# Performance work log

Measured on AMD Instinct MI355X. Metric: run time of the kernel, lower is better.

Reference implementation:

```python
import jax, jax.numpy as jnp
import numpy as np

NQ, BS, HW, D, H, DFF = 300, 16, 2048, 256, 8, 2048
HD2 = (2 * D) // H   # cross-attn head dim (query/key), 64
VHD = D // H         # value head dim, 32
EPS = 1e-5


def _lin_params(key, din, dout):
    kw, kb = jax.random.split(key)
    w = jax.random.normal(kw, (din, dout), jnp.float32) * 0.02
    b = jax.random.normal(kb, (dout,), jnp.float32) * 0.02
    return w, b


def setup_inputs() -> dict:
    key = jax.random.key(0)
    ks = jax.random.split(key, 24)
    inp = {
        'tgt': jax.random.normal(ks[0], (NQ, BS, D), jnp.float32),
        'memory': jax.random.normal(ks[1], (HW, BS, D), jnp.float32),
        'pos': jax.random.normal(ks[2], (HW, BS, D), jnp.float32),
        'cls_query_pos': jax.random.normal(ks[3], (NQ, BS, D), jnp.float32),
        'cls_query_sine_embed': jax.random.normal(ks[4], (NQ, BS, D), jnp.float32),
    }
    names = [('w_qc', 'b_qc', D, D), ('w_qp', 'b_qp', D, D), ('w_kc', 'b_kc', D, D),
             ('w_kp', 'b_kp', D, D), ('w_v', 'b_v', D, D), ('w_qs', 'b_qs', D, D),
             ('wq', 'bq', 2 * D, 2 * D), ('wk', 'bk', 2 * D, 2 * D),
             ('wv', 'bv', D, D), ('wo', 'bo', D, D),
             ('w1', 'b1', D, DFF), ('w2', 'b2', DFF, D)]
    for i, (wn, bn, din, dout) in enumerate(names):
        w, b = _lin_params(ks[5 + i], din, dout)
        inp[wn], inp[bn] = w, b
    inp['g2'] = jnp.ones((D,), jnp.float32)
    inp['be2'] = jnp.zeros((D,), jnp.float32)
    inp['g3'] = jnp.ones((D,), jnp.float32)
    inp['be3'] = jnp.zeros((D,), jnp.float32)
    return inp


def _ln(x, g, b):
    m = x.mean(-1, keepdims=True)
    v = ((x - m) ** 2).mean(-1, keepdims=True)
    return (x - m) * jax.lax.rsqrt(v + EPS) * g + b


def reference(tgt, memory, pos, cls_query_pos, cls_query_sine_embed,
              w_qc, b_qc, w_qp, b_qp, w_kc, b_kc, w_kp, b_kp, w_v, b_v,
              w_qs, b_qs, wq, bq, wk, bk, wv, bv, wo, bo,
              w1, b1, w2, b2, g2, be2, g3, be3):
    nq, bs, d = tgt.shape
    hw = memory.shape[0]
    # conditional cross-attention projections (is_first=True path)
    q_content = tgt @ w_qc + b_qc
    k_content = memory @ w_kc + b_kc
    v_in = memory @ w_v + b_v
    k_pos = pos @ w_kp + b_kp
    q_pos = cls_query_pos @ w_qp + b_qp
    q = (q_content + q_pos).reshape(nq, bs, H, d // H)
    sine = (cls_query_sine_embed @ w_qs + b_qs).reshape(nq, bs, H, d // H)
    q = jnp.concatenate([q, sine], axis=3).reshape(nq, bs, 2 * d)
    k = (k_content + k_pos).reshape(hw, bs, H, d // H)
    kp = k_pos.reshape(hw, bs, H, d // H)
    k = jnp.concatenate([k, kp], axis=3).reshape(hw, bs, 2 * d)
    # MultiheadAttention(embed_dim=2d, nhead, vdim=d): internal q/k/v/out projs
    scale = 1.0 / jnp.sqrt(jnp.float32(HD2))
    qh = ((q @ wq + bq) * scale).reshape(nq, bs, H, HD2)
    kh = (k @ wk + bk).reshape(hw, bs, H, HD2)
    vh = (v_in @ wv + bv).reshape(hw, bs, H, VHD)
    logits = jnp.einsum('qbhd,kbhd->bhqk', qh, kh)
    attn = jax.nn.softmax(logits, axis=-1)              # [bs, H, nq, hw]
    ctx = jnp.einsum('bhqk,kbhd->qbhd', attn, vh).reshape(nq, bs, d)
    tgt2 = ctx @ wo + bo
    attn_avg = attn.mean(axis=1)                        # averaged over heads
    # residual + norm + FFN + norm (dropout disabled / eval)
    x = _ln(tgt + tgt2, g2, be2)
    ffn = jax.nn.relu(x @ w1 + b1) @ w2 + b2
    x = _ln(x + ffn, g3, be3)
    return (x, attn_avg)
```

## Files before the change

### kernel.cpp

```cpp
#include <hip/hip_runtime.h>

typedef unsigned short u16;
typedef __attribute__((ext_vector_type(8))) short short8;
typedef __attribute__((ext_vector_type(4))) float f32x4;

#define MFMA16(a, b, c) __builtin_amdgcn_mfma_f32_16x16x32_bf16(a, b, c, 0, 0, 0)

__device__ __forceinline__ float bf2f(u16 u) {
    return __uint_as_float(((unsigned)u) << 16);
}
__device__ __forceinline__ u16 f2bf(float f) {
    unsigned u = __float_as_uint(f);
    u += 0x7fff + ((u >> 16) & 1);
    return (u16)(u >> 16);
}

__global__ __launch_bounds__(256) void cvt2(const float* __restrict__ a,
                                            const float* __restrict__ b,
                                            u16* __restrict__ A, u16* __restrict__ B) {
    size_t i = ((size_t)blockIdx.x * 256 + threadIdx.x) * 4;
    float4 va = *(const float4*)(a + i);
    float4 vb = *(const float4*)(b + i);
    u16 ta[4] = {f2bf(va.x), f2bf(va.y), f2bf(va.z), f2bf(va.w)};
    u16 tb[4] = {f2bf(vb.x), f2bf(vb.y), f2bf(vb.z), f2bf(vb.w)};
    *(uint2*)(A + i) = *(uint2*)ta;
    *(uint2*)(B + i) = *(uint2*)tb;
}


__global__ __launch_bounds__(256) void fold_q(const float* __restrict__ w_qc,
                                              const float* __restrict__ w_qp,
                                              const float* __restrict__ w_qs,
                                              const float* __restrict__ wq,
                                              u16* __restrict__ WQ3T) {
    int o = blockIdx.x * 256 + threadIdx.x;
    int k0 = blockIdx.y * 4;
    int seg = k0 >> 8, kb = k0 & 255;
    const float* wsrc = (seg == 0) ? w_qc : ((seg == 1) ? w_qp : w_qs);
    int sOff = (seg == 2) ? 32 : 0;
    const float* wcol = wq + o;
    float acc[4] = {0.f, 0.f, 0.f, 0.f};
#pragma unroll 8
    for (int c = 0; c < 256; c++) {
        int mc = (c >> 5) * 64 + (c & 31) + sOff;
        float w0 = wcol[(size_t)mc * 512];
#pragma unroll
        for (int j = 0; j < 4; j++)
            acc[j] += wsrc[(size_t)(kb + j) * 256 + c] * w0;
    }
    u16 outv[4];
#pragma unroll
    for (int j = 0; j < 4; j++) outv[j] = f2bf(acc[j] * 0.125f);
    *(uint2*)(WQ3T + (size_t)o * 768 + k0) = *(uint2*)outv;
}

__global__ __launch_bounds__(256) void fold_k(const float* __restrict__ w_kc,
                                              const float* __restrict__ w_kp,
                                              const float* __restrict__ wk,
                                              u16* __restrict__ WK2T) {
    int o = blockIdx.x * 256 + threadIdx.x;
    int k0 = blockIdx.y * 4;
    bool second = k0 >= 256;
    int kb = second ? k0 - 256 : k0;
    const float* wcol = wk + o;
    float acc[4] = {0.f, 0.f, 0.f, 0.f};
    if (second) {
#pragma unroll 8
        for (int c = 0; c < 256; c++) {
            int mc = (c >> 5) * 64 + (c & 31);
            float w0 = wcol[(size_t)mc * 512] + wcol[(size_t)(mc + 32) * 512];
#pragma unroll
            for (int j = 0; j < 4; j++)
                acc[j] += w_kp[(size_t)(kb + j) * 256 + c] * w0;
        }
    } else {
#pragma unroll 8
        for (int c = 0; c < 256; c++) {
            int mc = (c >> 5) * 64 + (c & 31);
            float w0 = wcol[(size_t)mc * 512];
#pragma unroll
            for (int j = 0; j < 4; j++)
                acc[j] += w_kc[(size_t)(kb + j) * 256 + c] * w0;
        }
    }
    u16 outv[4];
#pragma unroll
    for (int j = 0; j < 4; j++) outv[j] = f2bf(acc[j]);
    *(uint2*)(WK2T + (size_t)o * 512 + k0) = *(uint2*)outv;
}

__global__ __launch_bounds__(256) void fold_v(const float* __restrict__ w_v,
                                              const float* __restrict__ wv_w,
                                              u16* __restrict__ WV2T) {
    int o = threadIdx.x;
    int k0 = blockIdx.y * 4;
    float acc[4] = {0.f, 0.f, 0.f, 0.f};
#pragma unroll 8
    for (int c = 0; c < 256; c++) {
        float w0 = wv_w[(size_t)c * 256 + o];
#pragma unroll
        for (int j = 0; j < 4; j++)
            acc[j] += w_v[(size_t)(k0 + j) * 256 + c] * w0;
    }
    u16 outv[4];
#pragma unroll
    for (int j = 0; j < 4; j++) outv[j] = f2bf(acc[j]);
    *(uint2*)(WV2T + (size_t)o * 256 + k0) = *(uint2*)outv;
}

__global__ __launch_bounds__(256) void fold_bias(
    const float* b_qc, const float* b_qp, const float* b_qs, const float* wq, const float* bq,
    const float* b_kc, const float* b_kp, const float* wk, const float* bk,
    const float* b_v, const float* wv_w, const float* bv,
    float* BQF, float* BKF, float* BVF) {
    __shared__ float red[4][64];
    int tid = threadIdx.x, lane = tid & 63, wave = tid >> 6;
    int blk = blockIdx.x;
    float acc = 0.f;
    if (blk < 8) {
        int o = blk * 64 + lane;
#pragma unroll 4
        for (int c = wave * 64; c < wave * 64 + 64; c++) {
            int mc = (c >> 5) * 64 + (c & 31);
            acc += (b_qc[c] + b_qp[c]) * wq[(size_t)mc * 512 + o];
            acc += b_qs[c] * wq[(size_t)(mc + 32) * 512 + o];
        }
        red[wave][lane] = acc;
        __syncthreads();
        if (wave == 0)
            BQF[o] = (bq[o] + red[0][lane] + red[1][lane] + red[2][lane] + red[3][lane]) * 0.125f;
    } else if (blk < 16) {
        int o = (blk - 8) * 64 + lane;
#pragma unroll 4
        for (int c = wave * 64; c < wave * 64 + 64; c++) {
            int mc = (c >> 5) * 64 + (c & 31);
            acc += (b_kc[c] + b_kp[c]) * wk[(size_t)mc * 512 + o];
            acc += b_kp[c] * wk[(size_t)(mc + 32) * 512 + o];
        }
        red[wave][lane] = acc;
        __syncthreads();
        if (wave == 0)
            BKF[o] = bk[o] + red[0][lane] + red[1][lane] + red[2][lane] + red[3][lane];
    } else {
        int o = (blk - 16) * 64 + lane;
#pragma unroll 4
        for (int c = wave * 64; c < wave * 64 + 64; c++)
            acc += b_v[c] * wv_w[(size_t)c * 256 + o];
        red[wave][lane] = acc;
        __syncthreads();
        if (wave == 0)
            BVF[o] = bv[o] + red[0][lane] + red[1][lane] + red[2][lane] + red[3][lane];
    }
}

__global__ __launch_bounds__(256) void transpose_f2b(const float* __restrict__ src,
                                                     u16* __restrict__ dst, int R, int C) {
    __shared__ float tile[32][33];
    int c0 = blockIdx.x * 32, r0 = blockIdx.y * 32;
    int t = threadIdx.x;
    int j = t & 31, i0 = (t >> 5) * 4;
#pragma unroll
    for (int ii = 0; ii < 4; ii++)
        tile[i0 + ii][j] = src[(size_t)(r0 + i0 + ii) * C + c0 + j];
    __syncthreads();
    int i2 = t & 31, j0 = (t >> 5) * 4;
#pragma unroll
    for (int jj = 0; jj < 4; jj++)
        dst[(size_t)(c0 + j0 + jj) * R + r0 + i2] = f2bf(tile[i2][j0 + jj]);
}

#define APAD 40
__global__ __launch_bounds__(256) void gemm_bt(
    const void* __restrict__ A0v, const void* __restrict__ A1v, const void* __restrict__ A2v,
    int astride, int a_f32, const u16* __restrict__ BT, const float* __restrict__ bias,
    u16* __restrict__ C, int M, int N, int K, int mode) {
    __shared__ u16 As[128 * APAD];
    __shared__ u16 Bs[128 * APAD];
    int tid = threadIdx.x;
    int wave = tid >> 6, lane = tid & 63;
    int l15 = lane & 15, quad = lane >> 4;
    int wm = (wave >> 1) * 64, wn = (wave & 1) * 64;
    int gm0 = blockIdx.x * 128, gn0 = blockIdx.y * 128;
    f32x4 acc[4][4] = {};
    for (int k0 = 0; k0 < K; k0 += 32) {
        const void* ap;
        int kin;
        if (astride == 256) {
            int p = k0 >> 8;
            ap = (p == 0) ? A0v : ((p == 1) ? A1v : A2v);
            kin = k0 & 255;
        } else {
            ap = A0v;
            kin = k0;
        }
#pragma unroll
        for (int i = 0; i < 2; i++) {
            int idx = tid * 2 + i;
            int row = idx >> 2, seg = (idx & 3) * 8;
            int grow = gm0 + row;
            u16 tmp[8];
            if (a_f32) {
                float vv[8] = {0.f, 0.f, 0.f, 0.f, 0.f, 0.f, 0.f, 0.f};
                if (grow < M) {
                    const float* apf = (const float*)ap;
                    float4 u0 = *(const float4*)(apf + (size_t)grow * astride + kin + seg);
                    float4 u1 = *(const float4*)(apf + (size_t)grow * astride + kin + seg + 4);
                    vv[0] = u0.x; vv[1] = u0.y; vv[2] = u0.z; vv[3] = u0.w;
                    vv[4] = u1.x; vv[5] = u1.y; vv[6] = u1.z; vv[7] = u1.w;
                }
#pragma unroll
                for (int e = 0; e < 8; e++) tmp[e] = f2bf(vv[e]);
            } else {
                uint4 v;
                v.x = v.y = v.z = v.w = 0;
                if (grow < M) v = *(const uint4*)((const u16*)ap + (size_t)grow * astride + kin + seg);
                *(uint4*)tmp = v;
            }
            *(uint4*)(&As[row * APAD + seg]) = *(uint4*)tmp;
            int nrow = gn0 + row;
            uint4 w = *(const uint4*)(BT + (size_t)nrow * K + k0 + seg);
            *(uint4*)(&Bs[row * APAD + seg]) = w;
        }
        __syncthreads();
        short8 afr[4], bfr[4];
#pragma unroll
        for (int i = 0; i < 4; i++)
            afr[i] = *(const short8*)(&As[(wm + i * 16 + l15) * APAD + quad * 8]);
#pragma unroll
        for (int j = 0; j < 4; j++)
            bfr[j] = *(const short8*)(&Bs[(wn + j * 16 + l15) * APAD + quad * 8]);
#pragma unroll
        for (int i = 0; i < 4; i++)
#pragma unroll
            for (int j = 0; j < 4; j++) acc[i][j] = MFMA16(afr[i], bfr[j], acc[i][j]);
        __syncthreads();
    }
#pragma unroll
    for (int i = 0; i < 4; i++) {
        int row = gm0 + wm + i * 16 + quad * 4;
#pragma unroll
        for (int j = 0; j < 4; j++) {
            int col = gn0 + wn + j * 16 + l15;
            float bvv = bias[col];
#pragma unroll
            for (int r = 0; r < 4; r++) {
                int grow = row + r;
                if (grow < M) {
                    float v = acc[i][j][r] + bvv;
                    if (mode == 1) v = fmaxf(v, 0.f);
                    C[(size_t)grow * N + col] = f2bf(v);
                }
            }
        }
    }
}

__global__ __launch_bounds__(256) void attn_a(const u16* __restrict__ qh,
                                              const u16* __restrict__ kh,
                                              const u16* __restrict__ vhr,
                                              u16* __restrict__ ctxbuf,
                                              float* __restrict__ z8inv) {
    int qt = blockIdx.x, h = blockIdx.y, b = blockIdx.z;
    __shared__ u16 Qt[64 * 72];
    __shared__ u16 Kc[128 * 72];
    __shared__ u16 Pt[64 * 136];
    __shared__ u16 VTc[32 * 136];
    int tid = threadIdx.x, wave = tid >> 6, lane = tid & 63;
    int l15 = lane & 15, quad = lane >> 4;
    int q0 = qt * 64;
#pragma unroll
    for (int i = 0; i < 2; i++) {
        int idx = tid * 2 + i;
        int row = idx >> 3, seg = (idx & 7) * 8;
        uint4 v;
        v.x = v.y = v.z = v.w = 0;
        int q = q0 + row;
        if (q < 300) v = *(const uint4*)(qh + ((size_t)q * 16 + b) * 512 + h * 64 + seg);
        *(uint4*)(&Qt[row * 72 + seg]) = v;
    }
    const f32x4 zf = {0.f, 0.f, 0.f, 0.f};
    f32x4 cacc[2] = {};
    float zrow[4] = {0.f, 0.f, 0.f, 0.f};
    for (int kc0 = 0; kc0 < 2048; kc0 += 128) {
#pragma unroll
        for (int i = 0; i < 4; i++) {
            int idx = tid * 4 + i;
            int row = idx >> 3, seg = (idx & 7) * 8;
            *(uint4*)(&Kc[row * 72 + seg]) =
                *(const uint4*)(kh + ((size_t)(kc0 + row) * 16 + b) * 512 + h * 64 + seg);
        }
#pragma unroll
        for (int i = 0; i < 2; i++) {
            int idx = tid * 2 + i;
            int kk = idx >> 2, dseg = (idx & 3) * 8;
            u16 tmp[8];
            *(uint4*)tmp = *(const uint4*)(vhr + ((size_t)(kc0 + kk) * 16 + b) * 256 + h * 32 + dseg);
#pragma unroll
            for (int e = 0; e < 8; e++) VTc[(dseg + e) * 136 + kk] = tmp[e];
        }
        __syncthreads();
        f32x4 sacc[8];
#pragma unroll
        for (int t = 0; t < 8; t++) sacc[t] = zf;
#pragma unroll
        for (int d0 = 0; d0 < 64; d0 += 32) {
            short8 af = *(const short8*)(&Qt[(wave * 16 + l15) * 72 + d0 + quad * 8]);
#pragma unroll
            for (int t = 0; t < 8; t++) {
                short8 bf = *(const short8*)(&Kc[(t * 16 + l15) * 72 + d0 + quad * 8]);
                sacc[t] = MFMA16(af, bf, sacc[t]);
            }
        }
#pragma unroll
        for (int t = 0; t < 8; t++) {
#pragma unroll
            for (int r = 0; r < 4; r++) {
                float p = __expf(sacc[t][r]);
                zrow[r] += p;
                Pt[(wave * 16 + quad * 4 + r) * 136 + t * 16 + l15] = f2bf(p);
            }
        }
#pragma unroll
        for (int kk0 = 0; kk0 < 128; kk0 += 32) {
            short8 af = *(const short8*)(&Pt[(wave * 16 + l15) * 136 + kk0 + quad * 8]);
#pragma unroll
            for (int t = 0; t < 2; t++) {
                short8 bf = *(const short8*)(&VTc[(t * 16 + l15) * 136 + kk0 + quad * 8]);
                cacc[t] = MFMA16(af, bf, cacc[t]);
            }
        }
        __syncthreads();
    }
#pragma unroll
    for (int r = 0; r < 4; r++) {
        float z = zrow[r];
        z += __shfl_xor(z, 1);
        z += __shfl_xor(z, 2);
        z += __shfl_xor(z, 4);
        z += __shfl_xor(z, 8);
        zrow[r] = z;
    }
#pragma unroll
    for (int r = 0; r < 4; r++) {
        int q = q0 + wave * 16 + quad * 4 + r;
        if (q < 300) {
            float rz = 1.0f / zrow[r];
#pragma unroll
            for (int t = 0; t < 2; t++)
                ctxbuf[((size_t)q * 16 + b) * 256 + h * 32 + t * 16 + l15] = f2bf(cacc[t][r] * rz);
            if (l15 == 0) z8inv[((size_t)b * 8 + h) * 320 + q] = rz * 0.125f;
        }
    }
}

__global__ __launch_bounds__(256) void attn_b(const u16* __restrict__ qh,
                                              const u16* __restrict__ kh,
                                              const float* __restrict__ z8inv,
                                              float* __restrict__ out1) {
    int kc0 = blockIdx.x * 128, qt = blockIdx.y, b = blockIdx.z;
    __shared__ u16 Qt[64 * 72];
    __shared__ u16 Kc[128 * 72];
    int tid = threadIdx.x, wave = tid >> 6, lane = tid & 63;
    int l15 = lane & 15, quad = lane >> 4;
    int q0 = qt * 64;
    const f32x4 zf = {0.f, 0.f, 0.f, 0.f};
    float avg[8][4] = {};
    for (int h = 0; h < 8; h++) {
#pragma unroll
        for (int i = 0; i < 2; i++) {
            int idx = tid * 2 + i;
            int row = idx >> 3, seg = (idx & 7) * 8;
            uint4 v;
            v.x = v.y = v.z = v.w = 0;
            int q = q0 + row;
            if (q < 300) v = *(const uint4*)(qh + ((size_t)q * 16 + b) * 512 + h * 64 + seg);
            *(uint4*)(&Qt[row * 72 + seg]) = v;
        }
#pragma unroll
        for (int i = 0; i < 4; i++) {
            int idx = tid * 4 + i;
            int row = idx >> 3, seg = (idx & 7) * 8;
            *(uint4*)(&Kc[row * 72 + seg]) =
                *(const uint4*)(kh + ((size_t)(kc0 + row) * 16 + b) * 512 + h * 64 + seg);
        }
        __syncthreads();
        f32x4 sacc[8];
#pragma unroll
        for (int t = 0; t < 8; t++) sacc[t] = zf;
#pragma unroll
        for (int d0 = 0; d0 < 64; d0 += 32) {
            short8 af = *(const short8*)(&Qt[(wave * 16 + l15) * 72 + d0 + quad * 8]);
#pragma unroll
            for (int t = 0; t < 8; t++) {
                short8 bf = *(const short8*)(&Kc[(t * 16 + l15) * 72 + d0 + quad * 8]);
                sacc[t] = MFMA16(af, bf, sacc[t]);
            }
        }
        float zi[4];
#pragma unroll
        for (int r = 0; r < 4; r++) {
            int q = q0 + wave * 16 + quad * 4 + r;
            zi[r] = z8inv[((size_t)b * 8 + h) * 320 + (q < 319 ? q : 319)];
        }
#pragma unroll
        for (int t = 0; t < 8; t++)
#pragma unroll
            for (int r = 0; r < 4; r++) avg[t][r] += __expf(sacc[t][r]) * zi[r];
        __syncthreads();
    }
#pragma unroll
    for (int r = 0; r < 4; r++) {
        int q = q0 + wave * 16 + quad * 4 + r;
        if (q < 300) {
#pragma unroll
            for (int t = 0; t < 8; t++)
                out1[((size_t)b * 300 + q) * 2048 + kc0 + t * 16 + l15] = avg[t][r];
        }
    }
}

__global__ __launch_bounds__(256) void ln_kernel(const void* __restrict__ a, int a_f32,
                                                 const u16* __restrict__ bres,
                                                 const float* __restrict__ g,
                                                 const float* __restrict__ be,
                                                 void* __restrict__ out, int out_f32) {
    int row = blockIdx.x, t = threadIdx.x;
    float av = a_f32 ? ((const float*)a)[(size_t)row * 256 + t]
                     : bf2f(((const u16*)a)[(size_t)row * 256 + t]);
    float v = av + bf2f(bres[(size_t)row * 256 + t]);
    float s = v, sq = v * v;
#pragma unroll
    for (int o = 32; o; o >>= 1) {
        s += __shfl_xor(s, o);
        sq += __shfl_xor(sq, o);
    }
    __shared__ float red[8];
    int wave = t >> 6, lane = t & 63;
    if (lane == 0) {
        red[wave] = s;
        red[4 + wave] = sq;
    }
    __syncthreads();
    s = red[0] + red[1] + red[2] + red[3];
    sq = red[4] + red[5] + red[6] + red[7];
    float mean = s * (1.f / 256.f);
    float var = sq * (1.f / 256.f) - mean * mean;
    float rs = rsqrtf(var + 1e-5f);
    float res = (v - mean) * rs * g[t] + be[t];
    if (out_f32) ((float*)out)[(size_t)row * 256 + t] = res;
    else ((u16*)out)[(size_t)row * 256 + t] = f2bf(res);
}

extern "C" void kernel_launch(void* const* d_in, const int* in_sizes, int n_in,
                              void* d_out, int out_size, void* d_ws, size_t ws_size,
                              hipStream_t stream) {
    (void)in_sizes; (void)n_in; (void)out_size; (void)ws_size;
    const float* tgt = (const float*)d_in[0];
    const float* mem = (const float*)d_in[1];
    const float* pos = (const float*)d_in[2];
    const float* qpos = (const float*)d_in[3];
    const float* qsine = (const float*)d_in[4];
    const float* w_qc = (const float*)d_in[5];
    const float* b_qc = (const float*)d_in[6];
    const float* w_qp = (const float*)d_in[7];
    const float* b_qp = (const float*)d_in[8];
    const float* w_kc = (const float*)d_in[9];
    const float* b_kc = (const float*)d_in[10];
    const float* w_kp = (const float*)d_in[11];
    const float* b_kp = (const float*)d_in[12];
    const float* w_v = (const float*)d_in[13];
    const float* b_v = (const float*)d_in[14];
    const float* w_qs = (const float*)d_in[15];
    const float* b_qs = (const float*)d_in[16];
    const float* wq = (const float*)d_in[17];
    const float* bq = (const float*)d_in[18];
    const float* wk = (const float*)d_in[19];
    const float* bk = (const float*)d_in[20];
    const float* wv_w = (const float*)d_in[21];
    const float* bv = (const float*)d_in[22];
    const float* wo = (const float*)d_in[23];
    const float* bo = (const float*)d_in[24];
    const float* w1 = (const float*)d_in[25];
    const float* b1 = (const float*)d_in[26];
    const float* w2 = (const float*)d_in[27];
    const float* b2 = (const float*)d_in[28];
    const float* g2 = (const float*)d_in[29];
    const float* be2 = (const float*)d_in[30];
    const float* g3 = (const float*)d_in[31];
    const float* be3 = (const float*)d_in[32];

    char* ws = (char*)d_ws;
    u16* WQ3T = (u16*)(ws + 0x000000);
    u16* WK2T = (u16*)(ws + 0x0C0000);
    u16* WV2T = (u16*)(ws + 0x140000);
    u16* WOT  = (u16*)(ws + 0x160000);
    u16* W1T  = (u16*)(ws + 0x180000);
    u16* W2T  = (u16*)(ws + 0x280000);
    float* BQF = (float*)(ws + 0x380000);
    float* BKF = (float*)(ws + 0x381000);
    float* BVF = (float*)(ws + 0x382000);
    float* Z8  = (float*)(ws + 0x390000);
    u16* QH  = (u16*)(ws + 0x400000);
    u16* KH  = (u16*)(ws + 0x900000);
    u16* CTX = (u16*)(ws + 0x2900000);
    u16* TGT2 = (u16*)(ws + 0x900000);
    u16* XBUF = (u16*)(ws + 0xB60000);
    u16* FFNB = (u16*)(ws + 0xDC0000);
    u16* HBUF = (u16*)(ws + 0x1020000);

    float* out0 = (float*)d_out;
    float* out1 = out0 + 1228800;
    u16* MB  = (u16*)out1;
    u16* PB  = MB + 8388608;
    u16* VHR = PB;

    cvt2<<<8192, 256, 0, stream>>>(mem, pos, MB, PB);
    fold_q<<<dim3(2, 192), 256, 0, stream>>>(w_qc, w_qp, w_qs, wq, WQ3T);
    fold_k<<<dim3(2, 128), 256, 0, stream>>>(w_kc, w_kp, wk, WK2T);
    fold_v<<<dim3(1, 64), 256, 0, stream>>>(w_v, wv_w, WV2T);
    fold_bias<<<20, 256, 0, stream>>>(b_qc, b_qp, b_qs, wq, bq, b_kc, b_kp, wk, bk,
                                      b_v, wv_w, bv, BQF, BKF, BVF);
    transpose_f2b<<<dim3(8, 8), 256, 0, stream>>>(wo, WOT, 256, 256);
    transpose_f2b<<<dim3(64, 8), 256, 0, stream>>>(w1, W1T, 256, 2048);
    transpose_f2b<<<dim3(8, 64), 256, 0, stream>>>(w2, W2T, 2048, 256);

    gemm_bt<<<dim3(38, 4), 256, 0, stream>>>(tgt, qpos, qsine, 256, 1, WQ3T, BQF, QH, 4800, 512, 768, 0);
    gemm_bt<<<dim3(256, 4), 256, 0, stream>>>(MB, PB, nullptr, 256, 0, WK2T, BKF, KH, 32768, 512, 512, 0);
    gemm_bt<<<dim3(256, 2), 256, 0, stream>>>(MB, nullptr, nullptr, 256, 0, WV2T, BVF, VHR, 32768, 256, 256, 0);

    attn_a<<<dim3(5, 8, 16), 256, 0, stream>>>(QH, KH, VHR, CTX, Z8);
    attn_b<<<dim3(16, 5, 16), 256, 0, stream>>>(QH, KH, Z8, out1);

    gemm_bt<<<dim3(38, 2), 256, 0, stream>>>(CTX, nullptr, nullptr, 256, 0, WOT, bo, TGT2, 4800, 256, 256, 0);
    ln_kernel<<<4800, 256, 0, stream>>>(tgt, 1, TGT2, g2, be2, XBUF, 0);
    gemm_bt<<<dim3(38, 16), 256, 0, stream>>>(XBUF, nullptr, nullptr, 256, 0, W1T, b1, HBUF, 4800, 2048, 256, 1);
    gemm_bt<<<dim3(38, 2), 256, 0, stream>>>(HBUF, nullptr, nullptr, 2048, 0, W2T, b2, FFNB, 4800, 256, 2048, 0);
    ln_kernel<<<4800, 256, 0, stream>>>(XBUF, 0, FFNB, g3, be3, out0, 1);
}
```

Before: 589.9 us.

## Transpose attention MFMA operands for vectorized stores and swap GEMM grid axes

In both attention kernels the QK^T MFMA now takes K as the A operand and Q as the B operand. Each lane therefore holds four consecutive key columns for one query row. This lets attn_b write the head-averaged probabilities as float4 stores, and lets attn_a pack P into 8-byte LDS stores and keep a single row-sum that is shuffle-reduced across quads. Separately, the GEMM grid maps blockIdx.x to N tiles and blockIdx.y to M tiles, so consecutive blocks share the same A row tile and L2 reuse may improve. The change costs an extra shuffle to broadcast row sums when normalizing the context.

```diff
diff --git a/kernel.cpp b/kernel.cpp
--- a/kernel.cpp
+++ b/kernel.cpp
@@ -26,7 +26,6 @@
     *(uint2*)(A + i) = *(uint2*)ta;
     *(uint2*)(B + i) = *(uint2*)tb;
 }
-
 
 __global__ __launch_bounds__(256) void fold_q(const float* __restrict__ w_qc,
                                               const float* __restrict__ w_qp,
@@ -180,7 +179,7 @@
     int wave = tid >> 6, lane = tid & 63;
     int l15 = lane & 15, quad = lane >> 4;
     int wm = (wave >> 1) * 64, wn = (wave & 1) * 64;
-    int gm0 = blockIdx.x * 128, gn0 = blockIdx.y * 128;
+    int gm0 = blockIdx.y * 128, gn0 = blockIdx.x * 128;
     f32x4 acc[4][4] = {};
     for (int k0 = 0; k0 < K; k0 += 32) {
         const void* ap;
@@ -280,7 +279,7 @@
     }
     const f32x4 zf = {0.f, 0.f, 0.f, 0.f};
     f32x4 cacc[2] = {};
-    float zrow[4] = {0.f, 0.f, 0.f, 0.f};
+    float zl = 0.f;
     for (int kc0 = 0; kc0 < 2048; kc0 += 128) {
 #pragma unroll
         for (int i = 0; i < 4; i++) {
@@ -304,21 +303,23 @@
         for (int t = 0; t < 8; t++) sacc[t] = zf;
 #pragma unroll
         for (int d0 = 0; d0 < 64; d0 += 32) {
-            short8 af = *(const short8*)(&Qt[(wave * 16 + l15) * 72 + d0 + quad * 8]);
+            short8 bfq = *(const short8*)(&Qt[(wave * 16 + l15) * 72 + d0 + quad * 8]);
 #pragma unroll
             for (int t = 0; t < 8; t++) {
-                short8 bf = *(const short8*)(&Kc[(t * 16 + l15) * 72 + d0 + quad * 8]);
-                sacc[t] = MFMA16(af, bf, sacc[t]);
+                short8 afk = *(const short8*)(&Kc[(t * 16 + l15) * 72 + d0 + quad * 8]);
+                sacc[t] = MFMA16(afk, bfq, sacc[t]);
             }
         }
 #pragma unroll
         for (int t = 0; t < 8; t++) {
+            u16 pk[4];
 #pragma unroll
             for (int r = 0; r < 4; r++) {
                 float p = __expf(sacc[t][r]);
-                zrow[r] += p;
-                Pt[(wave * 16 + quad * 4 + r) * 136 + t * 16 + l15] = f2bf(p);
+                zl += p;
+                pk[r] = f2bf(p);
             }
+            *(uint2*)(&Pt[(wave * 16 + l15) * 136 + t * 16 + quad * 4]) = *(uint2*)pk;
         }
 #pragma unroll
         for (int kk0 = 0; kk0 < 128; kk0 += 32) {
@@ -331,24 +332,20 @@
         }
         __syncthreads();
     }
-#pragma unroll
-    for (int r = 0; r < 4; r++) {
-        float z = zrow[r];
-        z += __shfl_xor(z, 1);
-        z += __shfl_xor(z, 2);
-        z += __shfl_xor(z, 4);
-        z += __shfl_xor(z, 8);
-        zrow[r] = z;
+    zl += __shfl_xor(zl, 16);
+    zl += __shfl_xor(zl, 32);
+    {
+        int q = q0 + wave * 16 + l15;
+        if (quad == 0 && q < 300) z8inv[((size_t)b * 8 + h) * 320 + q] = 0.125f / zl;
     }
 #pragma unroll
     for (int r = 0; r < 4; r++) {
         int q = q0 + wave * 16 + quad * 4 + r;
         if (q < 300) {
-            float rz = 1.0f / zrow[r];
+            float rz = 1.0f / __shfl(zl, quad * 4 + r);
 #pragma unroll
             for (int t = 0; t < 2; t++)
                 ctxbuf[((size_t)q * 16 + b) * 256 + h * 32 + t * 16 + l15] = f2bf(cacc[t][r] * rz);
-            if (l15 == 0) z8inv[((size_t)b * 8 + h) * 320 + q] = rz * 0.125f;
         }
     }
 }
@@ -363,8 +360,9 @@
     int tid = threadIdx.x, wave = tid >> 6, lane = tid & 63;
     int l15 = lane & 15, quad = lane >> 4;
     int q0 = qt * 64;
+    int qme = q0 + wave * 16 + l15;
     const f32x4 zf = {0.f, 0.f, 0.f, 0.f};
-    float avg[8][4] = {};
+    f32x4 avg[8] = {};
     for (int h = 0; h < 8; h++) {
 #pragma unroll
         for (int i = 0; i < 2; i++) {
@@ -389,33 +387,25 @@
         for (int t = 0; t < 8; t++) sacc[t] = zf;
 #pragma unroll
         for (int d0 = 0; d0 < 64; d0 += 32) {
-            short8 af = *(const short8*)(&Qt[(wave * 16 + l15) * 72 + d0 + quad * 8]);
+            short8 bfq = *(const short8*)(&Qt[(wave * 16 + l15) * 72 + d0 + quad * 8]);
 #pragma unroll
             for (int t = 0; t < 8; t++) {
-                short8 bf = *(const short8*)(&Kc[(t * 16 + l15) * 72 + d0 + quad * 8]);
-                sacc[t] = MFMA16(af, bf, sacc[t]);
+                short8 afk = *(const short8*)(&Kc[(t * 16 + l15) * 72 + d0 + quad * 8]);
+                sacc[t] = MFMA16(afk, bfq, sacc[t]);
             }
         }
-        float zi[4];
-#pragma unroll
-        for (int r = 0; r < 4; r++) {
-            int q = q0 + wave * 16 + quad * 4 + r;
-            zi[r] = z8inv[((size_t)b * 8 + h) * 320 + (q < 319 ? q : 319)];
-        }
+        float zi = z8inv[((size_t)b * 8 + h) * 320 + (qme < 319 ? qme : 319)];
 #pragma unroll
         for (int t = 0; t < 8; t++)
 #pragma unroll
-            for (int r = 0; r < 4; r++) avg[t][r] += __expf(sacc[t][r]) * zi[r];
-        __syncthreads();
-    }
-#pragma unroll
-    for (int r = 0; r < 4; r++) {
-        int q = q0 + wave * 16 + quad * 4 + r;
-        if (q < 300) {
-#pragma unroll
-            for (int t = 0; t < 8; t++)
-                out1[((size_t)b * 300 + q) * 2048 + kc0 + t * 16 + l15] = avg[t][r];
-        }
+            for (int r = 0; r < 4; r++) avg[t][r] += __expf(sacc[t][r]) * zi;
+        __syncthreads();
+    }
+    if (qme < 300) {
+        float* op = out1 + ((size_t)b * 300 + qme) * 2048 + kc0 + quad * 4;
+#pragma unroll
+        for (int t = 0; t < 8; t++)
+            *(float4*)(op + t * 16) = *(float4*)(&avg[t]);
     }
 }
 
@@ -524,16 +514,16 @@
     transpose_f2b<<<dim3(64, 8), 256, 0, stream>>>(w1, W1T, 256, 2048);
     transpose_f2b<<<dim3(8, 64), 256, 0, stream>>>(w2, W2T, 2048, 256);
 
-    gemm_bt<<<dim3(38, 4), 256, 0, stream>>>(tgt, qpos, qsine, 256, 1, WQ3T, BQF, QH, 4800, 512, 768, 0);
-    gemm_bt<<<dim3(256, 4), 256, 0, stream>>>(MB, PB, nullptr, 256, 0, WK2T, BKF, KH, 32768, 512, 512, 0);
-    gemm_bt<<<dim3(256, 2), 256, 0, stream>>>(MB, nullptr, nullptr, 256, 0, WV2T, BVF, VHR, 32768, 256, 256, 0);
+    gemm_bt<<<dim3(4, 38), 256, 0, stream>>>(tgt, qpos, qsine, 256, 1, WQ3T, BQF, QH, 4800, 512, 768, 0);
+    gemm_bt<<<dim3(4, 256), 256, 0, stream>>>(MB, PB, nullptr, 256, 0, WK2T, BKF, KH, 32768, 512, 512, 0);
+    gemm_bt<<<dim3(2, 256), 256, 0, stream>>>(MB, nullptr, nullptr, 256, 0, WV2T, BVF, VHR, 32768, 256, 256, 0);
 
     attn_a<<<dim3(5, 8, 16), 256, 0, stream>>>(QH, KH, VHR, CTX, Z8);
     attn_b<<<dim3(16, 5, 16), 256, 0, stream>>>(QH, KH, Z8, out1);
 
-    gemm_bt<<<dim3(38, 2), 256, 0, stream>>>(CTX, nullptr, nullptr, 256, 0, WOT, bo, TGT2, 4800, 256, 256, 0);
+    gemm_bt<<<dim3(2, 38), 256, 0, stream>>>(CTX, nullptr, nullptr, 256, 0, WOT, bo, TGT2, 4800, 256, 256, 0);
     ln_kernel<<<4800, 256, 0, stream>>>(tgt, 1, TGT2, g2, be2, XBUF, 0);
-    gemm_bt<<<dim3(38, 16), 256, 0, stream>>>(XBUF, nullptr, nullptr, 256, 0, W1T, b1, HBUF, 4800, 2048, 256, 1);
-    gemm_bt<<<dim3(38, 2), 256, 0, stream>>>(HBUF, nullptr, nullptr, 2048, 0, W2T, b2, FFNB, 4800, 256, 2048, 0);
+    gemm_bt<<<dim3(16, 38), 256, 0, stream>>>(XBUF, nullptr, nullptr, 256, 0, W1T, b1, HBUF, 4800, 2048, 256, 1);
+    gemm_bt<<<dim3(2, 38), 256, 0, stream>>>(HBUF, nullptr, nullptr, 2048, 0, W2T, b2, FFNB, 4800, 256, 2048, 0);
     ln_kernel<<<4800, 256, 0, stream>>>(XBUF, 0, FFNB, g3, be3, out0, 1);
 }
```

New measurement: 603.9 us. 2.4% more time.
